# Performance work log

Measured on AMD Instinct MI355X. Metric: run time of the kernel, lower is better.

## Reference

```python
import jax, jax.numpy as jnp
import numpy as np

# db2 decomposition filters (pywt values); pytorch_wavelets reverses them and uses
# F.conv1d (cross-correlation), so we store the reversed filters.
_DEC_LO = np.array([-0.12940952255092145, 0.22414386804185735,
                    0.836516303737469, 0.48296291314469025])
_DEC_HI = np.array([-0.48296291314469025, 0.836516303737469,
                    -0.22414386804185735, 0.12940952255092145])
_H0 = jnp.asarray(_DEC_LO[::-1].copy(), dtype=jnp.float32)
_H1 = jnp.asarray(_DEC_HI[::-1].copy(), dtype=jnp.float32)


def _dwt_layer(x):
    """Vectorized equivalent of DWTLayer: db2 J=1 DWT along the channel axis at
    every (b,i,j) pixel, keeping first C//2 lo coeffs then first C//2 hi coeffs.
    pytorch_wavelets mode='zero' with L=4 and even C -> pad 2 each side, stride 2.
    x: [B, C, H, W] -> [B, C, H, W]
    """
    B, C, H, W = x.shape
    v = jnp.transpose(x, (0, 2, 3, 1)).reshape(B * H * W, 1, C)
    filt = jnp.stack([_H0, _H1])[:, None, :].astype(x.dtype)  # [2,1,4]
    out = jax.lax.conv_general_dilated(
        v, filt, window_strides=(2,), padding=((2, 2),),
        dimension_numbers=('NCH', 'OIH', 'NCH'))  # [BHW, 2, C//2 + 1]
    half = C // 2
    t = jnp.concatenate([out[:, 0, :half], out[:, 1, :half]], axis=-1)
    return jnp.transpose(t.reshape(B, H, W, C), (0, 3, 1, 2))


def setup_inputs() -> dict:
    key = jax.random.key(0)
    ks = jax.random.split(key, 7)
    B, C, H, W = 16, 360, 64, 64
    return {
        'x': jax.random.normal(ks[0], (B, C, H, W), dtype=jnp.float32),
        'conv_w': jax.random.normal(ks[1], (1, 1, 2, 7), dtype=jnp.float32) * 0.1,
        'conv_b': jax.random.normal(ks[2], (1,), dtype=jnp.float32) * 0.1,
        'w1': jax.random.normal(ks[3], (128, 90), dtype=jnp.float32) * 0.1,
        'b1': jax.random.normal(ks[4], (128,), dtype=jnp.float32) * 0.1,
        'w2': jax.random.normal(ks[5], (256, 128), dtype=jnp.float32) * 0.1,
        'b2': jax.random.normal(ks[6], (256,), dtype=jnp.float32) * 0.1,
    }


def reference(x, conv_w, conv_b, w1, b1, w2, b2):
    x = _dwt_layer(x)                     # [B,360,H,W]
    cd1 = x[:, 180:, :, :]                # detail half -> [B,180,H,W]
    cd1 = _dwt_layer(cd1)                 # [B,180,H,W]
    cd1 = cd1.reshape(-1, 1, 2, 90)       # torch .view(-1,2,90).unsqueeze(1)
    cd1 = jax.lax.conv_general_dilated(
        cd1, conv_w, window_strides=(1, 1), padding=((0, 0), (3, 3)),
        dimension_numbers=('NCHW', 'OIHW', 'NCHW'))
    cd1 = cd1 + conv_b[None, :, None, None]   # [N,1,1,90]
    cd1 = jax.nn.relu(cd1)
    cd1 = cd1.reshape(cd1.shape[0], 1, -1)    # [N,1,90]
    cd1 = jax.nn.relu(cd1 @ w1.T + b1)        # [N,1,128]
    out = cd1 @ w2.T + b2                     # [N,1,256]
    return out.reshape(-1, 256, 8, 8)
```

## Files before the change

kernel.cpp:

```cpp
#include <hip/hip_runtime.h>

using bf8   = __attribute__((ext_vector_type(8))) short;
using f32x4 = __attribute__((ext_vector_type(4))) float;

__device__ inline unsigned short f2bf(float f) {
  unsigned u = __float_as_uint(f);
  return (unsigned short)((u + 0x7FFFu + ((u >> 16) & 1u)) >> 16);
}
__device__ inline float bf2f(unsigned short h) {
  return __uint_as_float(((unsigned)h) << 16);
}

struct Gs { float g0[10]; float g1[10]; };
__host__ __device__ constexpr Gs make_g() {
  double H0[4] = {0.48296291314469025, 0.836516303737469,
                  0.22414386804185735, -0.12940952255092145};
  double H1[4] = {0.12940952255092145, -0.22414386804185735,
                  0.836516303737469, -0.48296291314469025};
  Gs r{};
  for (int d = 0; d < 10; ++d) {
    double a = 0.0, b = 0.0;
    for (int k = 0; k < 4; ++k) {
      int j = d - 2 * k;
      if (j >= 0 && j < 4) { a += H0[k] * H1[j]; b += H1[k] * H1[j]; }
    }
    r.g0[d] = (float)a; r.g1[d] = (float)b;
  }
  return r;
}

__global__ __launch_bounds__(256) void dwt2_kernel(const float* __restrict__ x,
                                                   unsigned short* __restrict__ A,
                                                   const float* __restrict__ w1,
                                                   const float* __restrict__ w2,
                                                   unsigned short* __restrict__ w1b,
                                                   unsigned short* __restrict__ w2b) {
  constexpr Gs G = make_g();
  const int bx = blockIdx.x;
  if (bx >= 512) {
    const int e = bx - 512;
#pragma unroll
    for (int t = 0; t < 4; ++t) {
      const int i = e * 1024 + t * 256 + threadIdx.x;
      if (i < 13312) {
        const int o = i / 104, k = i - 104 * o;
        w1b[i] = (k < 90) ? f2bf(w1[o * 90 + k]) : (unsigned short)0;
      } else {
        const int j = i - 13312;
        const int o = j / 136, k = j - 136 * o;
        w2b[j] = (k < 128) ? f2bf(w2[o * 128 + k]) : (unsigned short)0;
      }
    }
    return;
  }

  const int seg   = bx & 7;
  const int pb    = bx >> 3;
  const int b     = pb >> 2;
  const int chunk = pb & 3;
  const int s     = chunk * 1024 + 4 * threadIdx.x;

  const float4* xb = (const float4*)(x + (size_t)b * 360 * 4096 + s);
  unsigned short* Ab = A + (size_t)b * 180 * 4096 + s;

  const int c0 = (seg * 90) >> 3;
  const int c1 = ((seg + 1) * 90) >> 3;

  float4 w[10];
  const int base = 4 * c0 - 6;
#pragma unroll
  for (int i = 0; i < 10; ++i) {
    const int idx = base + i;
    w[i] = (idx >= 0) ? xb[(size_t)idx * 1024] : float4{0.f, 0.f, 0.f, 0.f};
  }

  for (int c = c0; c < c1; ++c) {
    float4 nx[4];
    const bool pf = (c + 1 < c1);
    const int nb = 4 * c + 4;
#pragma unroll
    for (int i = 0; i < 4; ++i)
      nx[i] = pf ? xb[(size_t)(nb + i) * 1024] : float4{0.f, 0.f, 0.f, 0.f};

    float4 lo{0.f, 0.f, 0.f, 0.f}, hi{0.f, 0.f, 0.f, 0.f};
#pragma unroll
    for (int d = 0; d < 10; ++d) {
      lo.x = fmaf(G.g0[d], w[d].x, lo.x);
      lo.y = fmaf(G.g0[d], w[d].y, lo.y);
      lo.z = fmaf(G.g0[d], w[d].z, lo.z);
      lo.w = fmaf(G.g0[d], w[d].w, lo.w);
      hi.x = fmaf(G.g1[d], w[d].x, hi.x);
      hi.y = fmaf(G.g1[d], w[d].y, hi.y);
      hi.z = fmaf(G.g1[d], w[d].z, hi.z);
      hi.w = fmaf(G.g1[d], w[d].w, hi.w);
    }
    *(ushort4*)&Ab[(size_t)c * 4096] =
        ushort4{f2bf(lo.x), f2bf(lo.y), f2bf(lo.z), f2bf(lo.w)};
    *(ushort4*)&Ab[(size_t)(c + 90) * 4096] =
        ushort4{f2bf(hi.x), f2bf(hi.y), f2bf(hi.z), f2bf(hi.w)};
#pragma unroll
    for (int i = 0; i < 6; ++i) w[i] = w[i + 4];
#pragma unroll
    for (int i = 0; i < 4; ++i) w[6 + i] = nx[i];
  }
}

__global__ __launch_bounds__(512, 1) void mlp_fused_kernel(
    const unsigned short* __restrict__ A,
    const float* __restrict__ cw, const float* __restrict__ cbp,
    const unsigned short* __restrict__ w1b,
    const unsigned short* __restrict__ w2b,
    const float* __restrict__ b1, const float* __restrict__ b2,
    float* __restrict__ out) {
  __shared__ unsigned short w1B[128 * 104];
  __shared__ unsigned short w2B[128 * 136];
  __shared__ unsigned short AsH[128 * 180];

  const int tid = threadIdx.x;
  const int fam = blockIdx.x & 1;
  const int cbk = blockIdx.x >> 1;

  {
    const uint4* s1 = (const uint4*)w1b;
    for (int i = tid; i < 1664; i += 512) ((uint4*)w1B)[i] = s1[i];
    const uint4* s2 = (const uint4*)(w2b + (size_t)fam * 128 * 136);
    for (int i = tid; i < 2176; i += 512) ((uint4*)w2B)[i] = s2[i];
  }

  float cwr[14];
#pragma unroll
  for (int k = 0; k < 14; ++k) cwr[k] = cw[k];
  const float cbv = cbp[0];

  const int w = tid >> 6, lane = tid & 63;
  const int l15 = lane & 15, q = lane >> 4;
  const int mrow = 16 * w + l15;

  float b1v[8], b2v[8];
#pragma unroll
  for (int nt = 0; nt < 8; ++nt) {
    b1v[nt] = b1[16 * nt + l15];
    b2v[nt] = b2[fam * 128 + 16 * nt + l15];
  }

  uint4 st[6];
  {
    const uint4* ns = (const uint4*)(A + (size_t)cbk * 128 * 180);
#pragma unroll
    for (int t = 0; t < 6; ++t) {
      const int idx = tid + 512 * t;
      if (idx < 2880) st[t] = ns[idx];
    }
  }

  for (int it = 0; it < 4; ++it) {
    const size_t g0 = (size_t)(cbk + 128 * it) * 128;

    __syncthreads();
#pragma unroll
    for (int t = 0; t < 6; ++t) {
      const int idx = tid + 512 * t;
      if (idx < 2880) ((uint4*)AsH)[idx] = st[t];
    }
    __syncthreads();

    if (it < 3) {
      const uint4* ns = (const uint4*)(A + (size_t)(cbk + 128 * (it + 1)) * 128 * 180);
#pragma unroll
      for (int t = 0; t < 6; ++t) {
        const int idx = tid + 512 * t;
        if (idx < 2880) st[t] = ns[idx];
      }
    }

    bf8 ya[3];
#pragma unroll
    for (int ks = 0; ks < 3; ++ks) {
      const int j0 = 32 * ks + 8 * q;
      float v0[14], v1[14];
#pragma unroll
      for (int t = 0; t < 14; ++t) {
        const int m = j0 - 3 + t;
        const bool ok = (m >= 0) && (m < 90);
        v0[t] = ok ? bf2f(AsH[mrow * 180 + m]) : 0.0f;
        v1[t] = ok ? bf2f(AsH[mrow * 180 + 90 + m]) : 0.0f;
      }
      bf8 r8;
#pragma unroll
      for (int d = 0; d < 8; ++d) {
        const int j = j0 + d;
        unsigned short rv = 0;
        if (j < 90) {
          float acc = cbv;
#pragma unroll
          for (int k = 0; k < 7; ++k) {
            acc = fmaf(v0[d + k], cwr[k], acc);
            acc = fmaf(v1[d + k], cwr[7 + k], acc);
          }
          rv = f2bf(fmaxf(acc, 0.0f));
        }
        r8[d] = (short)rv;
      }
      ya[ks] = r8;
    }

    f32x4 acc1[8];
#pragma unroll
    for (int nt = 0; nt < 8; ++nt) {
      f32x4 a = {0.f, 0.f, 0.f, 0.f};
#pragma unroll
      for (int ks = 0; ks < 3; ++ks) {
        const bf8 wb = *(const bf8*)&w1B[(16 * nt + l15) * 104 + 32 * ks + 8 * q];
        a = __builtin_amdgcn_mfma_f32_16x16x32_bf16(ya[ks], wb, a, 0, 0, 0);
      }
      acc1[nt] = a;
    }
    __syncthreads();

#pragma unroll
    for (int nt = 0; nt < 8; ++nt) {
#pragma unroll
      for (int r = 0; r < 4; ++r) {
        const int n = 16 * w + 4 * q + r;
        const int o = 16 * nt + l15;
        AsH[n * 136 + o] = f2bf(fmaxf(acc1[nt][r] + b1v[nt], 0.0f));
      }
    }

    bf8 ha[4];
#pragma unroll
    for (int ks = 0; ks < 4; ++ks)
      ha[ks] = *(const bf8*)&AsH[mrow * 136 + 32 * ks + 8 * q];

#pragma unroll 2
    for (int nt = 0; nt < 8; ++nt) {
      f32x4 a = {0.f, 0.f, 0.f, 0.f};
#pragma unroll
      for (int ks = 0; ks < 4; ++ks) {
        const bf8 wb = *(const bf8*)&w2B[(16 * nt + l15) * 136 + 32 * ks + 8 * q];
        a = __builtin_amdgcn_mfma_f32_16x16x32_bf16(ha[ks], wb, a, 0, 0, 0);
      }
#pragma unroll
      for (int r = 0; r < 4; ++r) {
        const int n = 16 * w + 4 * q + r;
        out[(g0 + n) * 256 + fam * 128 + 16 * nt + l15] = a[r] + b2v[nt];
      }
    }
  }
}

extern "C" void kernel_launch(void* const* d_in, const int* in_sizes, int n_in,
                              void* d_out, int out_size, void* d_ws, size_t ws_size,
                              hipStream_t stream) {
  const float* x  = (const float*)d_in[0];
  const float* cw = (const float*)d_in[1];
  const float* cb = (const float*)d_in[2];
  const float* w1 = (const float*)d_in[3];
  const float* b1 = (const float*)d_in[4];
  const float* w2 = (const float*)d_in[5];
  const float* b2 = (const float*)d_in[6];
  float* outp = (float*)d_out;

  unsigned short* Abf = (unsigned short*)d_ws;
  unsigned short* w1b = Abf + (size_t)16 * 180 * 4096;
  unsigned short* w2b = w1b + 13312;

  dwt2_kernel<<<559, 256, 0, stream>>>(x, Abf, w1, w2, w1b, w2b);
  mlp_fused_kernel<<<256, 512, 0, stream>>>(Abf, cw, cb, w1b, w2b, b1, b2, outp);
}
```

Before: 228.7 us.

## Replace LDS-staged persistent MLP kernel with direct global-read small-block kernel

The fused MLP kernel no longer stages the weights and activation tiles in shared memory across a persistent loop of 256 large blocks. It now launches 1024 blocks of 256 threads, each handling 64 rows and all 256 output columns. MFMA weight fragments and activation windows are read straight from global memory through the cache, with shared memory kept only for the hidden layer. This is meant to remove the per-block weight staging and barriers and to raise occupancy, at the cost of repeated global/L2 weight reads per block. The workspace layout is reordered so the weights come first.

```diff
diff --git a/kernel.cpp b/kernel.cpp
--- a/kernel.cpp
+++ b/kernel.cpp
@@ -2,6 +2,7 @@
 
 using bf8   = __attribute__((ext_vector_type(8))) short;
 using f32x4 = __attribute__((ext_vector_type(4))) float;
+typedef unsigned short u16x4 __attribute__((ext_vector_type(4)));
 
 __device__ inline unsigned short f2bf(float f) {
   unsigned u = __float_as_uint(f);
@@ -105,146 +106,108 @@
   }
 }
 
-__global__ __launch_bounds__(512, 1) void mlp_fused_kernel(
+__global__ __launch_bounds__(256, 4) void mlp_direct_kernel(
     const unsigned short* __restrict__ A,
     const float* __restrict__ cw, const float* __restrict__ cbp,
     const unsigned short* __restrict__ w1b,
     const unsigned short* __restrict__ w2b,
     const float* __restrict__ b1, const float* __restrict__ b2,
     float* __restrict__ out) {
-  __shared__ unsigned short w1B[128 * 104];
-  __shared__ unsigned short w2B[128 * 136];
-  __shared__ unsigned short AsH[128 * 180];
-
-  const int tid = threadIdx.x;
-  const int fam = blockIdx.x & 1;
-  const int cbk = blockIdx.x >> 1;
-
-  {
-    const uint4* s1 = (const uint4*)w1b;
-    for (int i = tid; i < 1664; i += 512) ((uint4*)w1B)[i] = s1[i];
-    const uint4* s2 = (const uint4*)(w2b + (size_t)fam * 128 * 136);
-    for (int i = tid; i < 2176; i += 512) ((uint4*)w2B)[i] = s2[i];
-  }
+  __shared__ unsigned short Hs[64 * 136];
+
+  const int tid  = threadIdx.x;
+  const int w    = tid >> 6, lane = tid & 63;
+  const int l15  = lane & 15, q = lane >> 4;
+  const int mrow = 16 * w + l15;
+  const size_t g0 = (size_t)blockIdx.x * 64;
 
   float cwr[14];
 #pragma unroll
   for (int k = 0; k < 14; ++k) cwr[k] = cw[k];
   const float cbv = cbp[0];
 
-  const int w = tid >> 6, lane = tid & 63;
-  const int l15 = lane & 15, q = lane >> 4;
-  const int mrow = 16 * w + l15;
-
-  float b1v[8], b2v[8];
+  float b1v[8], b2v[16];
+#pragma unroll
+  for (int nt = 0; nt < 8; ++nt) b1v[nt] = b1[16 * nt + l15];
+#pragma unroll
+  for (int nt = 0; nt < 16; ++nt) b2v[nt] = b2[16 * nt + l15];
+
+  const unsigned short* Ar = A + (size_t)(g0 + mrow) * 180;
+  bf8 ya[3];
+#pragma unroll
+  for (int ks = 0; ks < 3; ++ks) {
+    const int j0 = 32 * ks + 8 * q;
+    u16x4 L[4], Hc[5];
+#pragma unroll
+    for (int k = 0; k < 4; ++k) L[k] = *(const u16x4*)(Ar + j0 - 4 + 4 * k);
+#pragma unroll
+    for (int k = 0; k < 5; ++k) Hc[k] = *(const u16x4*)(Ar + j0 + 84 + 4 * k);
+
+    float v0[14], v1[14];
+#pragma unroll
+    for (int t = 0; t < 14; ++t) {
+      const int m = j0 - 3 + t;
+      const bool ok = (m >= 0) && (m < 90);
+      v0[t] = ok ? bf2f((unsigned short)L[(t + 1) >> 2][(t + 1) & 3]) : 0.0f;
+      v1[t] = ok ? bf2f((unsigned short)Hc[(t + 3) >> 2][(t + 3) & 3]) : 0.0f;
+    }
+    bf8 r8;
+#pragma unroll
+    for (int d = 0; d < 8; ++d) {
+      const int j = j0 + d;
+      unsigned short rv = 0;
+      if (j < 90) {
+        float acc = cbv;
+#pragma unroll
+        for (int k = 0; k < 7; ++k) {
+          acc = fmaf(v0[d + k], cwr[k], acc);
+          acc = fmaf(v1[d + k], cwr[7 + k], acc);
+        }
+        rv = f2bf(fmaxf(acc, 0.0f));
+      }
+      r8[d] = (short)rv;
+    }
+    ya[ks] = r8;
+  }
+
+  f32x4 acc1[8];
 #pragma unroll
   for (int nt = 0; nt < 8; ++nt) {
-    b1v[nt] = b1[16 * nt + l15];
-    b2v[nt] = b2[fam * 128 + 16 * nt + l15];
-  }
-
-  uint4 st[6];
-  {
-    const uint4* ns = (const uint4*)(A + (size_t)cbk * 128 * 180);
-#pragma unroll
-    for (int t = 0; t < 6; ++t) {
-      const int idx = tid + 512 * t;
-      if (idx < 2880) st[t] = ns[idx];
-    }
-  }
-
-  for (int it = 0; it < 4; ++it) {
-    const size_t g0 = (size_t)(cbk + 128 * it) * 128;
-
-    __syncthreads();
-#pragma unroll
-    for (int t = 0; t < 6; ++t) {
-      const int idx = tid + 512 * t;
-      if (idx < 2880) ((uint4*)AsH)[idx] = st[t];
-    }
-    __syncthreads();
-
-    if (it < 3) {
-      const uint4* ns = (const uint4*)(A + (size_t)(cbk + 128 * (it + 1)) * 128 * 180);
-#pragma unroll
-      for (int t = 0; t < 6; ++t) {
-        const int idx = tid + 512 * t;
-        if (idx < 2880) st[t] = ns[idx];
-      }
-    }
-
-    bf8 ya[3];
+    f32x4 a = {0.f, 0.f, 0.f, 0.f};
 #pragma unroll
     for (int ks = 0; ks < 3; ++ks) {
-      const int j0 = 32 * ks + 8 * q;
-      float v0[14], v1[14];
-#pragma unroll
-      for (int t = 0; t < 14; ++t) {
-        const int m = j0 - 3 + t;
-        const bool ok = (m >= 0) && (m < 90);
-        v0[t] = ok ? bf2f(AsH[mrow * 180 + m]) : 0.0f;
-        v1[t] = ok ? bf2f(AsH[mrow * 180 + 90 + m]) : 0.0f;
-      }
-      bf8 r8;
-#pragma unroll
-      for (int d = 0; d < 8; ++d) {
-        const int j = j0 + d;
-        unsigned short rv = 0;
-        if (j < 90) {
-          float acc = cbv;
-#pragma unroll
-          for (int k = 0; k < 7; ++k) {
-            acc = fmaf(v0[d + k], cwr[k], acc);
-            acc = fmaf(v1[d + k], cwr[7 + k], acc);
-          }
-          rv = f2bf(fmaxf(acc, 0.0f));
-        }
-        r8[d] = (short)rv;
-      }
-      ya[ks] = r8;
-    }
-
-    f32x4 acc1[8];
-#pragma unroll
-    for (int nt = 0; nt < 8; ++nt) {
-      f32x4 a = {0.f, 0.f, 0.f, 0.f};
-#pragma unroll
-      for (int ks = 0; ks < 3; ++ks) {
-        const bf8 wb = *(const bf8*)&w1B[(16 * nt + l15) * 104 + 32 * ks + 8 * q];
-        a = __builtin_amdgcn_mfma_f32_16x16x32_bf16(ya[ks], wb, a, 0, 0, 0);
-      }
-      acc1[nt] = a;
-    }
-    __syncthreads();
-
-#pragma unroll
-    for (int nt = 0; nt < 8; ++nt) {
-#pragma unroll
-      for (int r = 0; r < 4; ++r) {
-        const int n = 16 * w + 4 * q + r;
-        const int o = 16 * nt + l15;
-        AsH[n * 136 + o] = f2bf(fmaxf(acc1[nt][r] + b1v[nt], 0.0f));
-      }
-    }
-
-    bf8 ha[4];
-#pragma unroll
-    for (int ks = 0; ks < 4; ++ks)
-      ha[ks] = *(const bf8*)&AsH[mrow * 136 + 32 * ks + 8 * q];
-
-#pragma unroll 2
-    for (int nt = 0; nt < 8; ++nt) {
-      f32x4 a = {0.f, 0.f, 0.f, 0.f};
-#pragma unroll
-      for (int ks = 0; ks < 4; ++ks) {
-        const bf8 wb = *(const bf8*)&w2B[(16 * nt + l15) * 136 + 32 * ks + 8 * q];
-        a = __builtin_amdgcn_mfma_f32_16x16x32_bf16(ha[ks], wb, a, 0, 0, 0);
-      }
-#pragma unroll
-      for (int r = 0; r < 4; ++r) {
-        const int n = 16 * w + 4 * q + r;
-        out[(g0 + n) * 256 + fam * 128 + 16 * nt + l15] = a[r] + b2v[nt];
-      }
+      const bf8 wb = *(const bf8*)&w1b[(16 * nt + l15) * 104 + 32 * ks + 8 * q];
+      a = __builtin_amdgcn_mfma_f32_16x16x32_bf16(ya[ks], wb, a, 0, 0, 0);
+    }
+    acc1[nt] = a;
+  }
+
+#pragma unroll
+  for (int nt = 0; nt < 8; ++nt) {
+#pragma unroll
+    for (int r = 0; r < 4; ++r) {
+      const int n = 16 * w + 4 * q + r;
+      Hs[n * 136 + 16 * nt + l15] = f2bf(fmaxf(acc1[nt][r] + b1v[nt], 0.0f));
+    }
+  }
+
+  bf8 ha[4];
+#pragma unroll
+  for (int ks = 0; ks < 4; ++ks)
+    ha[ks] = *(const bf8*)&Hs[mrow * 136 + 32 * ks + 8 * q];
+
+#pragma unroll 4
+  for (int nt = 0; nt < 16; ++nt) {
+    f32x4 a = {0.f, 0.f, 0.f, 0.f};
+#pragma unroll
+    for (int ks = 0; ks < 4; ++ks) {
+      const bf8 wb = *(const bf8*)&w2b[(16 * nt + l15) * 136 + 32 * ks + 8 * q];
+      a = __builtin_amdgcn_mfma_f32_16x16x32_bf16(ha[ks], wb, a, 0, 0, 0);
+    }
+#pragma unroll
+    for (int r = 0; r < 4; ++r) {
+      const int n = 16 * w + 4 * q + r;
+      out[(g0 + n) * 256 + 16 * nt + l15] = a[r] + b2v[nt];
     }
   }
 }
@@ -261,10 +224,10 @@
   const float* b2 = (const float*)d_in[6];
   float* outp = (float*)d_out;
 
-  unsigned short* Abf = (unsigned short*)d_ws;
-  unsigned short* w1b = Abf + (size_t)16 * 180 * 4096;
+  unsigned short* w1b = (unsigned short*)d_ws;
   unsigned short* w2b = w1b + 13312;
+  unsigned short* Abf = w1b + 48128;
 
   dwt2_kernel<<<559, 256, 0, stream>>>(x, Abf, w1, w2, w1b, w2b);
-  mlp_fused_kernel<<<256, 512, 0, stream>>>(Abf, cw, cb, w1b, w2b, b1, b2, outp);
-}
+  mlp_direct_kernel<<<1024, 256, 0, stream>>>(Abf, cw, cb, w1b, w2b, b1, b2, outp);
+}
```

Measured after the change: 198.9 us. -13.0%, faster.
